# Performance work log

Hardware: AMD Instinct MI355X
Metric: run time of the kernel (lower is better)

## Reference

```python
import jax, jax.numpy as jnp
import numpy as np
import math

B, N, DIM, DEPTH, HEADS, DHEAD = 4, 8192, 256, 4, 8, 32
NB = int(DHEAD * math.log(DHEAD))  # 110 random features (performer_pytorch default)
INNER = HEADS * DHEAD  # 256


def _ortho_proj(rng, nb, d):
    # gaussian orthogonal random matrix, scaling=0 (row norms of a fresh gaussian)
    blocks = []
    for _ in range(-(-nb // d)):
        q, _ = np.linalg.qr(rng.standard_normal((d, d)))
        blocks.append(q.T)
    m = np.concatenate(blocks, 0)[:nb]
    mult = np.linalg.norm(rng.standard_normal((nb, d)), axis=1)
    return (mult[:, None] * m).astype(np.float32)


def setup_inputs() -> dict:
    rng = np.random.default_rng(0)
    p = lambda *s: jnp.asarray((rng.standard_normal(s) * 0.02).astype(np.float32))
    return {
        "x": jnp.asarray(rng.standard_normal((B, N, DIM)).astype(np.float32)),
        "proj": jnp.asarray(np.stack([_ortho_proj(rng, NB, DHEAD) for _ in range(DEPTH)])),
        "ln1_g": jnp.ones((DEPTH, DIM), jnp.float32),
        "ln1_b": jnp.zeros((DEPTH, DIM), jnp.float32),
        "Wq": p(DEPTH, DIM, INNER), "bq": jnp.zeros((DEPTH, INNER), jnp.float32),
        "Wk": p(DEPTH, DIM, INNER), "bk": jnp.zeros((DEPTH, INNER), jnp.float32),
        "Wv": p(DEPTH, DIM, INNER), "bv": jnp.zeros((DEPTH, INNER), jnp.float32),
        "Wo": p(DEPTH, INNER, DIM), "bo": jnp.zeros((DEPTH, DIM), jnp.float32),
        "ln2_g": jnp.ones((DEPTH, DIM), jnp.float32),
        "ln2_b": jnp.zeros((DEPTH, DIM), jnp.float32),
        "Wf1": p(DEPTH, DIM, 4 * DIM), "bf1": jnp.zeros((DEPTH, 4 * DIM), jnp.float32),
        "Wf2": p(DEPTH, 4 * DIM, DIM), "bf2": jnp.zeros((DEPTH, DIM), jnp.float32),
    }


def _ln(x, g, b):
    m = jnp.mean(x, axis=-1, keepdims=True)
    v = jnp.var(x, axis=-1, keepdims=True)
    return (x - m) * jax.lax.rsqrt(v + 1e-5) * g + b


def _softmax_kernel(x, proj, is_query, eps=1e-4):
    # FAVOR+ positive softmax-kernel feature map
    dn = x.shape[-1] ** -0.25
    ratio = proj.shape[0] ** -0.5
    xd = jnp.einsum('bhnd,md->bhnm', x * dn, proj)          # [b,h,n,nb]
    diag = jnp.sum(x * x, axis=-1, keepdims=True) * (0.5 * dn * dn)
    if is_query:
        mx = jnp.max(xd, axis=-1, keepdims=True)
    else:
        mx = jnp.max(xd, axis=(-2, -1), keepdims=True)
    mx = jax.lax.stop_gradient(mx)
    return ratio * (jnp.exp(xd - diag - mx) + eps)


def reference(x, proj, ln1_g, ln1_b, Wq, bq, Wk, bk, Wv, bv, Wo, bo,
              ln2_g, ln2_b, Wf1, bf1, Wf2, bf2):
    b, n, _ = x.shape
    h = x
    for i in range(DEPTH):
        # --- PreNorm FAVOR+ self-attention ---
        y = _ln(h, ln1_g[i], ln1_b[i])
        q = (y @ Wq[i] + bq[i]).reshape(b, n, HEADS, DHEAD).transpose(0, 2, 1, 3)
        k = (y @ Wk[i] + bk[i]).reshape(b, n, HEADS, DHEAD).transpose(0, 2, 1, 3)
        v = (y @ Wv[i] + bv[i]).reshape(b, n, HEADS, DHEAD).transpose(0, 2, 1, 3)
        qp = _softmax_kernel(q, proj[i], True)   # [b,h,n,nb]
        kp = _softmax_kernel(k, proj[i], False)  # [b,h,n,nb]
        d_inv = 1.0 / jnp.einsum('bhnm,bhm->bhn', qp, kp.sum(axis=2))
        ctx = jnp.einsum('bhnm,bhnd->bhmd', kp, v)          # [b,h,nb,d]
        o = jnp.einsum('bhnm,bhmd,bhn->bhnd', qp, ctx, d_inv)
        o = o.transpose(0, 2, 1, 3).reshape(b, n, INNER)
        h = h + o @ Wo[i] + bo[i]
        # --- PreNorm FFN ---
        y = _ln(h, ln2_g[i], ln2_b[i])
        h = h + jax.nn.gelu(y @ Wf1[i] + bf1[i]) @ Wf2[i] + bf2[i]
    return h
```

## Files before the change

### kernel.cpp

```cpp
#include <hip/hip_runtime.h>
#include <math.h>

#define NSEQ 8192
#define BATCH 4
#define DIM 256
#define HEADS 8
#define DHEAD 32
#define NB 110
#define INNER 256
#define FFDIM 1024
#define MROWS (BATCH * NSEQ)
#define BH (BATCH * HEADS)

typedef __attribute__((ext_vector_type(8))) short bf16x8;
typedef __attribute__((ext_vector_type(4))) short bf16x4;
typedef __attribute__((ext_vector_type(4))) float f32x4;

typedef __attribute__((address_space(1))) const void* gas_cvp;
typedef __attribute__((address_space(3))) void* las_vp;

constexpr float c_dn = 0.42044820762685725f;
constexpr float c_diagf = 0.08838834764831845f;
constexpr float c_ratio = 0.09534625892455922f;

__device__ __forceinline__ unsigned short f2b(float f) {
    unsigned u = __float_as_uint(f);
    unsigned r = (u + 0x7FFFu + ((u >> 16) & 1u)) >> 16;
    return (unsigned short)r;
}
__device__ __forceinline__ float b2f(unsigned short u) {
    return __uint_as_float((unsigned)u << 16);
}

__global__ __launch_bounds__(256) void copy4_kernel(const float4* __restrict__ src,
                                                    float4* __restrict__ dst, int n4) {
    int i = blockIdx.x * 256 + threadIdx.x;
    if (i < n4) dst[i] = src[i];
}
__global__ __launch_bounds__(256) void zero_kernel(float* __restrict__ p, int n) {
    int i = blockIdx.x * 256 + threadIdx.x;
    if (i < n) p[i] = 0.0f;
}
__global__ __launch_bounds__(256) void bcat_kernel(const float* __restrict__ bq,
                                                   const float* __restrict__ bk,
                                                   const float* __restrict__ bv,
                                                   float* __restrict__ out) {
    int l = blockIdx.x, t = threadIdx.x;
    out[l * 768 + t] = bq[l * 256 + t];
    out[l * 768 + 256 + t] = bk[l * 256 + t];
    out[l * 768 + 512 + t] = bv[l * 256 + t];
}

__global__ __launch_bounds__(256) void ln_kernel(const float* __restrict__ x,
                                                 const float* __restrict__ g,
                                                 const float* __restrict__ bta,
                                                 unsigned short* __restrict__ y) {
    int wave = threadIdx.x >> 6, lane = threadIdx.x & 63;
    int row = blockIdx.x * 4 + wave;
    const float* xr = x + (size_t)row * DIM;
    float4 v = *(const float4*)(xr + lane * 4);
    float s = v.x + v.y + v.z + v.w;
    float sq = v.x * v.x + v.y * v.y + v.z * v.z + v.w * v.w;
    #pragma unroll
    for (int off = 32; off; off >>= 1) {
        s += __shfl_xor(s, off);
        sq += __shfl_xor(sq, off);
    }
    float mean = s * (1.0f / DIM);
    float var = sq * (1.0f / DIM) - mean * mean;
    float rstd = rsqrtf(var + 1e-5f);
    float4 gg = *(const float4*)(g + lane * 4);
    float4 bb = *(const float4*)(bta + lane * 4);
    bf16x4 o;
    o[0] = (short)f2b((v.x - mean) * rstd * gg.x + bb.x);
    o[1] = (short)f2b((v.y - mean) * rstd * gg.y + bb.y);
    o[2] = (short)f2b((v.z - mean) * rstd * gg.z + bb.z);
    o[3] = (short)f2b((v.w - mean) * rstd * gg.w + bb.w);
    *(bf16x4*)(y + (size_t)row * DIM + lane * 4) = o;
}

__global__ __launch_bounds__(256) void wt_kernel(const float* __restrict__ in,
                                                 unsigned short* __restrict__ out,
                                                 int K, int Nn, int lstride) {
    __shared__ float t32[32][33];
    int l = blockIdx.z;
    const float* inp = in + (size_t)l * K * Nn;
    unsigned short* outp = out + (size_t)l * lstride;
    int k0 = blockIdx.x * 32, n0 = blockIdx.y * 32;
    int tx = threadIdx.x & 31, ty = threadIdx.x >> 5;
    #pragma unroll
    for (int i = 0; i < 4; ++i)
        t32[ty + i * 8][tx] = inp[(size_t)(k0 + ty + i * 8) * Nn + n0 + tx];
    __syncthreads();
    #pragma unroll
    for (int i = 0; i < 4; ++i) {
        int r = ty + i * 8;
        outp[(size_t)(n0 + r) * K + k0 + tx] = f2b(t32[tx][r]);
    }
}

template <int EPI>
__global__ __launch_bounds__(256) void gemm_mfma(const unsigned short* __restrict__ A,
                                                 const unsigned short* __restrict__ Wt,
                                                 const float* __restrict__ bias,
                                                 const float* __restrict__ res,
                                                 void* __restrict__ Cv,
                                                 int Nn, int K) {
    __shared__ __align__(16) unsigned short pool[24576];
    unsigned short* AsP = pool;
    unsigned short* BsP = pool + 12288;
    int tid = threadIdx.x;
    int nwg = gridDim.x * gridDim.y;
    int orig = blockIdx.y * gridDim.x + blockIdx.x;
    int swz = (orig & 7) * (nwg >> 3) + (orig >> 3);
    int m0 = (swz / gridDim.x) * 128, n0 = (swz % gridDim.x) * 128;
    int wave = tid >> 6, lane = tid & 63;
    int wm = (wave >> 1) * 64, wn = (wave & 1) * 64;
    int lr = lane & 15, lg = lane >> 4;
    f32x4 acc[4][4];
    #pragma unroll
    for (int i = 0; i < 4; ++i)
        #pragma unroll
        for (int j = 0; j < 4; ++j) acc[i][j] = (f32x4){0.f, 0.f, 0.f, 0.f};

    int rowS[2], chS[2];
    #pragma unroll
    for (int j = 0; j < 2; ++j) {
        int f = wave * 128 + j * 64 + lane;
        rowS[j] = f >> 2;
        chS[j] = ((f & 3) ^ ((rowS[j] >> 1) & 3)) * 8;
    }
    int rdA[4], rdB[4];
    #pragma unroll
    for (int i = 0; i < 4; ++i) {
        int ra = wm + i * 16 + lr;
        rdA[i] = ra * 32 + (lg ^ ((ra >> 1) & 3)) * 8;
        int rb = wn + i * 16 + lr;
        rdB[i] = rb * 32 + (lg ^ ((rb >> 1) & 3)) * 8;
    }

    const int NT = K >> 5;
    #pragma unroll
    for (int t = 0; t < 2; ++t) {
        #pragma unroll
        for (int j = 0; j < 2; ++j) {
            const unsigned short* srcA = A + (size_t)(m0 + rowS[j]) * K + t * 32 + chS[j];
            __builtin_amdgcn_global_load_lds((gas_cvp)srcA,
                                             (las_vp)(AsP + t * 4096 + wave * 1024 + j * 512), 16, 0, 0);
            const unsigned short* srcB = Wt + (size_t)(n0 + rowS[j]) * K + t * 32 + chS[j];
            __builtin_amdgcn_global_load_lds((gas_cvp)srcB,
                                             (las_vp)(BsP + t * 4096 + wave * 1024 + j * 512), 16, 0, 0);
        }
    }
    int buf = 0;
    for (int kt = 0; kt < NT; ++kt) {
        if (kt + 2 < NT) {
            int nb = (kt + 2) % 3;
            int koff = (kt + 2) * 32;
            #pragma unroll
            for (int j = 0; j < 2; ++j) {
                const unsigned short* srcA = A + (size_t)(m0 + rowS[j]) * K + koff + chS[j];
                __builtin_amdgcn_global_load_lds((gas_cvp)srcA,
                                                 (las_vp)(AsP + nb * 4096 + wave * 1024 + j * 512), 16, 0, 0);
                const unsigned short* srcB = Wt + (size_t)(n0 + rowS[j]) * K + koff + chS[j];
                __builtin_amdgcn_global_load_lds((gas_cvp)srcB,
                                                 (las_vp)(BsP + nb * 4096 + wave * 1024 + j * 512), 16, 0, 0);
            }
        }
        int ahead = NT - 1 - kt;
        if (ahead >= 2)      asm volatile("s_waitcnt vmcnt(8)" ::: "memory");
        else if (ahead == 1) asm volatile("s_waitcnt vmcnt(4)" ::: "memory");
        else                 asm volatile("s_waitcnt vmcnt(0)" ::: "memory");
        __builtin_amdgcn_s_barrier();
        __builtin_amdgcn_sched_barrier(0);
        bf16x8 af[4], bfv[4];
        #pragma unroll
        for (int i = 0; i < 4; ++i) af[i] = *(bf16x8*)&AsP[buf * 4096 + rdA[i]];
        #pragma unroll
        for (int j = 0; j < 4; ++j) bfv[j] = *(bf16x8*)&BsP[buf * 4096 + rdB[j]];
        #pragma unroll
        for (int i = 0; i < 4; ++i)
            #pragma unroll
            for (int j = 0; j < 4; ++j)
                acc[i][j] = __builtin_amdgcn_mfma_f32_16x16x32_bf16(af[i], bfv[j], acc[i][j], 0, 0, 0);
        __builtin_amdgcn_sched_barrier(0);
        __builtin_amdgcn_s_barrier();
        buf = (buf + 1 == 3) ? 0 : buf + 1;
    }

    #pragma unroll
    for (int i = 0; i < 4; ++i) {
        #pragma unroll
        for (int j = 0; j < 4; ++j) {
            int tcol = wn + j * 16 + lr;
            float bv = bias[n0 + tcol];
            #pragma unroll
            for (int r = 0; r < 4; ++r) {
                int trow = wm + i * 16 + lg * 4 + r;
                float c = acc[i][j][r] + bv;
                if (EPI == 2) {
                    float u = c;
                    float t = 1.5957691216057308f * (u + 0.044715f * u * u * u);
                    c = u / (1.0f + __expf(-t));
                }
                pool[trow * 128 + (((tcol >> 3) ^ (trow & 7)) << 3) + (tcol & 7)] = f2b(c);
            }
        }
    }
    __syncthreads();
    #pragma unroll
    for (int cch = 0; cch < 8; ++cch) {
        int g = cch * 256 + tid;
        int row = g >> 4, cc = g & 15;
        bf16x8 val = *(bf16x8*)&pool[row * 128 + ((cc ^ (row & 7)) << 3)];
        int grow = m0 + row;
        int gcol = n0 + cc * 8;
        if (EPI == 3) {
            size_t idx = (size_t)(gcol >> 8) * ((size_t)MROWS * DIM) + (size_t)grow * 256 + (gcol & 255);
            *(bf16x8*)((unsigned short*)Cv + idx) = val;
        } else {
            *(bf16x8*)((unsigned short*)Cv + (size_t)grow * Nn + gcol) = val;
        }
    }
}

template <int DO_LN>
__global__ __launch_bounds__(256) void gemm_ln(const unsigned short* __restrict__ A,
                                               const unsigned short* __restrict__ Wt,
                                               const float* __restrict__ bias,
                                               const float* __restrict__ res,
                                               float* __restrict__ hout,
                                               unsigned short* __restrict__ yout,
                                               const float* __restrict__ gam,
                                               const float* __restrict__ bet,
                                               int K) {
    __shared__ __align__(16) unsigned short As[2][64 * 32];
    __shared__ __align__(16) unsigned short Bs[2][256 * 32];
    int tid = threadIdx.x;
    int nwg = gridDim.y;
    int orig = blockIdx.y;
    int swz = (orig & 7) * (nwg >> 3) + (orig >> 3);
    int m0 = swz * 64;
    int wave = tid >> 6, lane = tid & 63;
    int lr = lane & 15, lg = lane >> 4;

    f32x4 acc[16];
    #pragma unroll
    for (int j = 0; j < 16; ++j) acc[j] = (f32x4){0.f, 0.f, 0.f, 0.f};

    int fA = wave * 64 + lane;
    int rowA = fA >> 2, chA = ((fA & 3) ^ ((rowA >> 1) & 3)) * 8;
    int rowB[4], chB[4];
    #pragma unroll
    for (int j = 0; j < 4; ++j) {
        int f = wave * 256 + j * 64 + lane;
        rowB[j] = f >> 2;
        chB[j] = ((f & 3) ^ ((rowB[j] >> 1) & 3)) * 8;
    }
    int raA = wave * 16 + lr;
    int rdAo = raA * 32 + (lg ^ ((raA >> 1) & 3)) * 8;
    int rdBo[16];
    #pragma unroll
    for (int j = 0; j < 16; ++j) {
        int rb = j * 16 + lr;
        rdBo[j] = rb * 32 + (lg ^ ((rb >> 1) & 3)) * 8;
    }

    const int NT = K >> 5;
    {
        const unsigned short* srcA = A + (size_t)(m0 + rowA) * K + chA;
        __builtin_amdgcn_global_load_lds((gas_cvp)srcA, (las_vp)(&As[0][wave * 512]), 16, 0, 0);
        #pragma unroll
        for (int j = 0; j < 4; ++j) {
            const unsigned short* srcB = Wt + (size_t)rowB[j] * K + chB[j];
            __builtin_amdgcn_global_load_lds((gas_cvp)srcB, (las_vp)(&Bs[0][wave * 2048 + j * 512]), 16, 0, 0);
        }
    }
    for (int kt = 0; kt < NT; ++kt) {
        int cur = kt & 1;
        if (kt + 1 < NT) {
            int nxt = cur ^ 1;
            int koff = (kt + 1) * 32;
            const unsigned short* srcA = A + (size_t)(m0 + rowA) * K + koff + chA;
            __builtin_amdgcn_global_load_lds((gas_cvp)srcA, (las_vp)(&As[nxt][wave * 512]), 16, 0, 0);
            #pragma unroll
            for (int j = 0; j < 4; ++j) {
                const unsigned short* srcB = Wt + (size_t)rowB[j] * K + koff + chB[j];
                __builtin_amdgcn_global_load_lds((gas_cvp)srcB, (las_vp)(&Bs[nxt][wave * 2048 + j * 512]), 16, 0, 0);
            }
            asm volatile("s_waitcnt vmcnt(5)" ::: "memory");
        } else {
            asm volatile("s_waitcnt vmcnt(0)" ::: "memory");
        }
        __builtin_amdgcn_s_barrier();
        __builtin_amdgcn_sched_barrier(0);
        bf16x8 af = *(bf16x8*)&As[cur][rdAo];
        #pragma unroll
        for (int j = 0; j < 16; ++j) {
            bf16x8 bv = *(bf16x8*)&Bs[cur][rdBo[j]];
            acc[j] = __builtin_amdgcn_mfma_f32_16x16x32_bf16(af, bv, acc[j], 0, 0, 0);
        }
        __builtin_amdgcn_sched_barrier(0);
        __builtin_amdgcn_s_barrier();
    }

    float rs[4] = {0.f, 0.f, 0.f, 0.f};
    float rq[4] = {0.f, 0.f, 0.f, 0.f};
    #pragma unroll
    for (int j = 0; j < 16; ++j) {
        int col = j * 16 + lr;
        float bv = bias[col];
        #pragma unroll
        for (int r = 0; r < 4; ++r) {
            int row = m0 + wave * 16 + lg * 4 + r;
            float c = acc[j][r] + bv + res[(size_t)row * 256 + col];
            hout[(size_t)row * 256 + col] = c;
            acc[j][r] = c;
            if (DO_LN) { rs[r] += c; rq[r] += c * c; }
        }
    }
    if (DO_LN) {
        #pragma unroll
        for (int r = 0; r < 4; ++r) {
            float s = rs[r], sq = rq[r];
            s += __shfl_xor(s, 1);  sq += __shfl_xor(sq, 1);
            s += __shfl_xor(s, 2);  sq += __shfl_xor(sq, 2);
            s += __shfl_xor(s, 4);  sq += __shfl_xor(sq, 4);
            s += __shfl_xor(s, 8);  sq += __shfl_xor(sq, 8);
            rs[r] = s; rq[r] = sq;
        }
        #pragma unroll
        for (int r = 0; r < 4; ++r) {
            float mean = rs[r] * (1.0f / 256.0f);
            float var = rq[r] * (1.0f / 256.0f) - mean * mean;
            rs[r] = mean;
            rq[r] = rsqrtf(var + 1e-5f);
        }
        #pragma unroll
        for (int j = 0; j < 16; ++j) {
            int col = j * 16 + lr;
            float gv = gam[col], bb = bet[col];
            #pragma unroll
            for (int r = 0; r < 4; ++r) {
                int row = m0 + wave * 16 + lg * 4 + r;
                float yv = (acc[j][r] - rs[r]) * rq[r] * gv + bb;
                yout[(size_t)row * 256 + col] = f2b(yv);
            }
        }
    }
}

__global__ __launch_bounds__(256) void kmaxg_kernel(const unsigned short* __restrict__ k,
                                                    const float* __restrict__ proj,
                                                    float* __restrict__ partial) {
    __shared__ unsigned short As[128][40];
    __shared__ unsigned short Pj[112][40];
    __shared__ float wmax[4][8];
    int tid = threadIdx.x;
    int r0 = blockIdx.x * 128;
    for (int idx = tid; idx < 112 * 8; idx += 256) {
        int m = idx >> 3, f4 = idx & 7;
        if (m < NB) {
            float4 va = *(const float4*)(proj + m * 32 + f4 * 4);
            bf16x4 pk = {(short)f2b(va.x), (short)f2b(va.y), (short)f2b(va.z), (short)f2b(va.w)};
            *(bf16x4*)&Pj[m][f4 * 4] = pk;
        } else {
            *(bf16x4*)&Pj[m][f4 * 4] = (bf16x4){0, 0, 0, 0};
        }
    }
    int arow = tid >> 1, ahalf = tid & 1;
    const unsigned short* ap = k + (size_t)(r0 + arow) * 32 + ahalf * 16;
    *(bf16x8*)&As[arow][ahalf * 16] = *(const bf16x8*)ap;
    *(bf16x8*)&As[arow][ahalf * 16 + 8] = *(const bf16x8*)(ap + 8);
    __syncthreads();
    int wave = tid >> 6, lane = tid & 63, lr = lane & 15, lg = lane >> 4;
    float mymax[4] = {-1e30f, -1e30f, -1e30f, -1e30f};
    #pragma unroll
    for (int mt = 0; mt < 2; ++mt) {
        bf16x8 af = *(bf16x8*)&As[(2 * wave + mt) * 16 + lr][lg * 8];
        #pragma unroll
        for (int nt = 0; nt < 7; ++nt) {
            bf16x8 bfp = *(bf16x8*)&Pj[nt * 16 + lr][lg * 8];
            f32x4 d = (f32x4){0.f, 0.f, 0.f, 0.f};
            d = __builtin_amdgcn_mfma_f32_16x16x32_bf16(af, bfp, d, 0, 0, 0);
            if (!(nt == 6 && lr >= 14)) {
                #pragma unroll
                for (int r = 0; r < 4; ++r) mymax[r] = fmaxf(mymax[r], d[r]);
            }
        }
    }
    #pragma unroll
    for (int r = 0; r < 4; ++r) {
        float v = mymax[r];
        v = fmaxf(v, __shfl_xor(v, 1));
        v = fmaxf(v, __shfl_xor(v, 2));
        v = fmaxf(v, __shfl_xor(v, 4));
        v = fmaxf(v, __shfl_xor(v, 8));
        v = fmaxf(v, __shfl_xor(v, 32));
        mymax[r] = v;
    }
    if (lane == 0 || lane == 16) {
        int hb = (lane >> 4) & 1;
        #pragma unroll
        for (int r = 0; r < 4; ++r) wmax[wave][4 * hb + r] = mymax[r];
    }
    __syncthreads();
    if (tid < 8) {
        float m = fmaxf(fmaxf(wmax[0][tid], wmax[1][tid]), fmaxf(wmax[2][tid], wmax[3][tid]));
        partial[blockIdx.x * 8 + tid] = m * c_dn;
    }
}

__global__ __launch_bounds__(256) void kreduce_kernel(const float* __restrict__ partial,
                                                      float* __restrict__ kmaxf) {
    __shared__ float wred[4];
    int bh = blockIdx.x, b = bh >> 3, h = bh & 7;
    int tid = threadIdx.x;
    float m = fmaxf(partial[(b * 512 + tid) * 8 + h], partial[(b * 512 + 256 + tid) * 8 + h]);
    #pragma unroll
    for (int off = 32; off; off >>= 1) m = fmaxf(m, __shfl_xor(m, off));
    if ((tid & 63) == 0) wred[tid >> 6] = m;
    __syncthreads();
    if (tid == 0)
        kmaxf[bh] = fmaxf(fmaxf(wred[0], wred[1]), fmaxf(wred[2], wred[3]));
}

__global__ __launch_bounds__(256) void ctxg_kernel(const unsigned short* __restrict__ k,
                                                   const unsigned short* __restrict__ v,
                                                   const float* __restrict__ proj,
                                                   const float* __restrict__ kmaxf,
                                                   float* __restrict__ ctx) {
    __shared__ __align__(16) char pool[34816];
    unsigned short (*As)[40] = (unsigned short(*)[40])pool;
    unsigned short (*KpT)[136] = (unsigned short(*)[136])pool;
    __shared__ unsigned short Pj[112][40];
    __shared__ unsigned short VsT[48][136];
    __shared__ float dg[128];
    int tid = threadIdx.x;
    int bh = blockIdx.y, b = bh >> 3, h = bh & 7;
    int n_base = blockIdx.x * 512;
    float mx = kmaxf[bh];
    for (int idx = tid; idx < 112 * 8; idx += 256) {
        int m = idx >> 3, f4 = idx & 7;
        if (m < NB) {
            float4 va = *(const float4*)(proj + m * 32 + f4 * 4);
            bf16x4 pk = {(short)f2b(va.x), (short)f2b(va.y), (short)f2b(va.z), (short)f2b(va.w)};
            *(bf16x4*)&Pj[m][f4 * 4] = pk;
        } else {
            *(bf16x4*)&Pj[m][f4 * 4] = (bf16x4){0, 0, 0, 0};
        }
    }
    for (int idx = tid; idx < 16 * 136; idx += 256) KpT[112 + idx / 136][idx % 136] = 0;
    for (int idx = tid; idx < 16 * 128; idx += 256) {
        int rr = 32 + (idx >> 7), nn = idx & 127;
        VsT[rr][nn] = (rr == 32) ? (unsigned short)0x3F80 : (unsigned short)0;
    }
    int wave = tid >> 6, lane = tid & 63, lr = lane & 15, lg = lane >> 4;
    int arow = tid >> 1, ahalf = tid & 1;
    f32x4 ctxacc[2][3];
    #pragma unroll
    for (int mt = 0; mt < 2; ++mt)
        #pragma unroll
        for (int nt = 0; nt < 3; ++nt) ctxacc[mt][nt] = (f32x4){0.f, 0.f, 0.f, 0.f};

    for (int ni = 0; ni < 4; ++ni) {
        int n0 = n_base + ni * 128;
        {
            const unsigned short* kp_ = k + ((size_t)(b * NSEQ + n0 + arow) * 256 + h * 32 + ahalf * 16);
            bf16x8 k0 = *(const bf16x8*)kp_;
            bf16x8 k1 = *(const bf16x8*)(kp_ + 8);
            *(bf16x8*)&As[arow][ahalf * 16] = k0;
            *(bf16x8*)&As[arow][ahalf * 16 + 8] = k1;
            float ssq = 0.f;
            #pragma unroll
            for (int e = 0; e < 8; ++e) {
                float a = b2f((unsigned short)k0[e]), bb = b2f((unsigned short)k1[e]);
                ssq += a * a + bb * bb;
            }
            ssq += __shfl_xor(ssq, 1);
            if (ahalf == 0) dg[arow] = ssq * c_diagf;
        }
        #pragma unroll
        for (int it = 0; it < 4; ++it) {
            int idx = it * 256 + tid;
            int nn = idx >> 3, f4 = idx & 7;
            bf16x4 vv = *(const bf16x4*)(v + ((size_t)(b * NSEQ + n0 + nn) * 256 + h * 32 + f4 * 4));
            VsT[f4 * 4 + 0][nn] = (unsigned short)vv[0];
            VsT[f4 * 4 + 1][nn] = (unsigned short)vv[1];
            VsT[f4 * 4 + 2][nn] = (unsigned short)vv[2];
            VsT[f4 * 4 + 3][nn] = (unsigned short)vv[3];
        }
        __syncthreads();
        f32x4 xds[2][7];
        #pragma unroll
        for (int mt = 0; mt < 2; ++mt) {
            bf16x8 af = *(bf16x8*)&As[(2 * wave + mt) * 16 + lr][lg * 8];
            #pragma unroll
            for (int nt = 0; nt < 7; ++nt) {
                bf16x8 bfp = *(bf16x8*)&Pj[nt * 16 + lr][lg * 8];
                f32x4 d = (f32x4){0.f, 0.f, 0.f, 0.f};
                xds[mt][nt] = __builtin_amdgcn_mfma_f32_16x16x32_bf16(af, bfp, d, 0, 0, 0);
            }
        }
        __syncthreads();
        #pragma unroll
        for (int mt = 0; mt < 2; ++mt)
            #pragma unroll
            for (int nt = 0; nt < 7; ++nt) {
                int m = nt * 16 + lr;
                #pragma unroll
                for (int r = 0; r < 4; ++r) {
                    int nn = (2 * wave + mt) * 16 + lg * 4 + r;
                    float kpv = (m < NB) ? c_ratio * (__expf(xds[mt][nt][r] * c_dn - dg[nn] - mx) + 1e-4f) : 0.f;
                    KpT[m][nn] = f2b(kpv);
                }
            }
        __syncthreads();
        #pragma unroll
        for (int ks = 0; ks < 4; ++ks)
            #pragma unroll
            for (int mt = 0; mt < 2; ++mt) {
                bf16x8 af2 = *(bf16x8*)&KpT[(2 * wave + mt) * 16 + lr][ks * 32 + lg * 8];
                #pragma unroll
                for (int nt = 0; nt < 3; ++nt) {
                    bf16x8 bf2v = *(bf16x8*)&VsT[nt * 16 + lr][ks * 32 + lg * 8];
                    ctxacc[mt][nt] = __builtin_amdgcn_mfma_f32_16x16x32_bf16(af2, bf2v, ctxacc[mt][nt], 0, 0, 0);
                }
            }
        __syncthreads();
    }
    #pragma unroll
    for (int mt = 0; mt < 2; ++mt)
        #pragma unroll
        for (int nt = 0; nt < 3; ++nt)
            #pragma unroll
            for (int r = 0; r < 4; ++r) {
                int m = (2 * wave + mt) * 16 + lg * 4 + r;
                atomicAdd(&ctx[((size_t)bh * 128 + m) * 48 + nt * 16 + lr], ctxacc[mt][nt][r]);
            }
}

__global__ __launch_bounds__(256) void og_kernel(const unsigned short* __restrict__ q,
                                                 const float* __restrict__ proj,
                                                 const float* __restrict__ ctx,
                                                 unsigned short* __restrict__ o) {
    __shared__ __align__(16) char pool[34816];
    unsigned short (*As)[40] = (unsigned short(*)[40])pool;
    unsigned short (*Qp)[136] = (unsigned short(*)[136])pool;
    __shared__ unsigned short Pj[112][40];
    __shared__ unsigned short CsT[48][136];
    __shared__ float dg[128];
    int tid = threadIdx.x;
    int bh = blockIdx.x >> 6, b = bh >> 3, h = bh & 7;
    int n0 = (blockIdx.x & 63) * 128;
    for (int idx = tid; idx < 112 * 8; idx += 256) {
        int m = idx >> 3, f4 = idx & 7;
        if (m < NB) {
            float4 va = *(const float4*)(proj + m * 32 + f4 * 4);
            bf16x4 pk = {(short)f2b(va.x), (short)f2b(va.y), (short)f2b(va.z), (short)f2b(va.w)};
            *(bf16x4*)&Pj[m][f4 * 4] = pk;
        } else {
            *(bf16x4*)&Pj[m][f4 * 4] = (bf16x4){0, 0, 0, 0};
        }
    }
    for (int idx = tid; idx < 128 * 12; idx += 256) {
        int m = idx / 12, c4 = idx - m * 12;
        float4 cv = *(const float4*)(ctx + ((size_t)bh * 128 + m) * 48 + c4 * 4);
        CsT[c4 * 4 + 0][m] = f2b(cv.x);
        CsT[c4 * 4 + 1][m] = f2b(cv.y);
        CsT[c4 * 4 + 2][m] = f2b(cv.z);
        CsT[c4 * 4 + 3][m] = f2b(cv.w);
    }
    int arow = tid >> 1, ahalf = tid & 1;
    {
        const unsigned short* qp_ = q + ((size_t)(b * NSEQ + n0 + arow) * 256 + h * 32 + ahalf * 16);
        bf16x8 q0 = *(const bf16x8*)qp_;
        bf16x8 q1 = *(const bf16x8*)(qp_ + 8);
        *(bf16x8*)&As[arow][ahalf * 16] = q0;
        *(bf16x8*)&As[arow][ahalf * 16 + 8] = q1;
        float ssq = 0.f;
        #pragma unroll
        for (int e = 0; e < 8; ++e) {
            float a = b2f((unsigned short)q0[e]), bb = b2f((unsigned short)q1[e]);
            ssq += a * a + bb * bb;
        }
        ssq += __shfl_xor(ssq, 1);
        if (ahalf == 0) dg[arow] = ssq * c_diagf;
    }
    __syncthreads();
    int wave = tid >> 6, lane = tid & 63, lr = lane & 15, lg = lane >> 4;
    f32x4 xds[2][7];
    #pragma unroll
    for (int mt = 0; mt < 2; ++mt) {
        bf16x8 af = *(bf16x8*)&As[(2 * wave + mt) * 16 + lr][lg * 8];
        #pragma unroll
        for (int nt = 0; nt < 7; ++nt) {
            bf16x8 bfp = *(bf16x8*)&Pj[nt * 16 + lr][lg * 8];
            f32x4 d = (f32x4){0.f, 0.f, 0.f, 0.f};
            xds[mt][nt] = __builtin_amdgcn_mfma_f32_16x16x32_bf16(af, bfp, d, 0, 0, 0);
        }
    }
    float rmax[2][4];
    #pragma unroll
    for (int mt = 0; mt < 2; ++mt)
        #pragma unroll
        for (int r = 0; r < 4; ++r) {
            float mv = -1e30f;
            #pragma unroll
            for (int nt = 0; nt < 7; ++nt)
                if (!(nt == 6 && lr >= 14)) mv = fmaxf(mv, xds[mt][nt][r]);
            mv = fmaxf(mv, __shfl_xor(mv, 1));
            mv = fmaxf(mv, __shfl_xor(mv, 2));
            mv = fmaxf(mv, __shfl_xor(mv, 4));
            mv = fmaxf(mv, __shfl_xor(mv, 8));
            rmax[mt][r] = mv;
        }
    __syncthreads();
    #pragma unroll
    for (int mt = 0; mt < 2; ++mt)
        #pragma unroll
        for (int r = 0; r < 4; ++r) {
            int row = (2 * wave + mt) * 16 + lg * 4 + r;
            #pragma unroll
            for (int nt = 0; nt < 7; ++nt) {
                int m = nt * 16 + lr;
                float qpv = (m < NB)
                    ? c_ratio * (__expf((xds[mt][nt][r] - rmax[mt][r]) * c_dn - dg[row]) + 1e-4f)
                    : 0.f;
                Qp[row][m] = f2b(qpv);
            }
            Qp[row][112 + lr] = 0;
        }
    __syncthreads();
    f32x4 oacc[2][3];
    #pragma unroll
    for (int mt = 0; mt < 2; ++mt)
        #pragma unroll
        for (int nt = 0; nt < 3; ++nt) oacc[mt][nt] = (f32x4){0.f, 0.f, 0.f, 0.f};
    #pragma unroll
    for (int ks = 0; ks < 4; ++ks)
        #pragma unroll
        for (int mt = 0; mt < 2; ++mt) {
            bf16x8 af2 = *(bf16x8*)&Qp[(2 * wave + mt) * 16 + lr][ks * 32 + lg * 8];
            #pragma unroll
            for (int nt = 0; nt < 3; ++nt) {
                bf16x8 bf2v = *(bf16x8*)&CsT[nt * 16 + lr][ks * 32 + lg * 8];
                oacc[mt][nt] = __builtin_amdgcn_mfma_f32_16x16x32_bf16(af2, bf2v, oacc[mt][nt], 0, 0, 0);
            }
        }
    #pragma unroll
    for (int mt = 0; mt < 2; ++mt)
        #pragma unroll
        for (int r = 0; r < 4; ++r) {
            int row = (2 * wave + mt) * 16 + lg * 4 + r;
            int n = n0 + row;
            float den = __shfl(oacc[mt][2][r], lane & 48);
            float inv = 1.0f / den;
            size_t base = (size_t)(b * NSEQ + n) * 256 + h * 32;
            o[base + lr] = f2b(oacc[mt][0][r] * inv);
            o[base + 16 + lr] = f2b(oacc[mt][1][r] * inv);
        }
}

extern "C" void kernel_launch(void* const* d_in, const int* in_sizes, int n_in,
                              void* d_out, int out_size, void* d_ws, size_t ws_size,
                              hipStream_t stream) {
    const float* x = (const float*)d_in[0];
    const float* proj = (const float*)d_in[1];
    const float* ln1_g = (const float*)d_in[2];
    const float* ln1_b = (const float*)d_in[3];
    const float* Wq = (const float*)d_in[4];
    const float* bq = (const float*)d_in[5];
    const float* Wk = (const float*)d_in[6];
    const float* bk = (const float*)d_in[7];
    const float* Wv = (const float*)d_in[8];
    const float* bv = (const float*)d_in[9];
    const float* Wo = (const float*)d_in[10];
    const float* bo = (const float*)d_in[11];
    const float* ln2_g = (const float*)d_in[12];
    const float* ln2_b = (const float*)d_in[13];
    const float* Wf1 = (const float*)d_in[14];
    const float* bf1 = (const float*)d_in[15];
    const float* Wf2 = (const float*)d_in[16];
    const float* bf2 = (const float*)d_in[17];

    float* h = (float*)d_out;
    const size_t ACT = (size_t)MROWS * DIM;
    unsigned short* y = (unsigned short*)d_ws;
    unsigned short* q = y + ACT;
    unsigned short* k = q + ACT;
    unsigned short* v = k + ACT;
    unsigned short* mid = v + ACT;
    float* ctx = (float*)(mid + 4 * ACT);
    float* kmaxf = ctx + (size_t)BH * 128 * 48;
    float* partial = kmaxf + 32;
    float* bqkv = partial + 2048 * 8;
    unsigned short* wt = (unsigned short*)(bqkv + 4 * 768);
    unsigned short* o = y;

    const int WT_L = 786432;
    const int CTXN = BH * 128 * 48;

    copy4_kernel<<<(int)(ACT / 4) / 256, 256, 0, stream>>>((const float4*)x, (float4*)h, (int)(ACT / 4));

    wt_kernel<<<dim3(8, 8, 4), 256, 0, stream>>>(Wq, wt + 0, 256, 256, WT_L);
    wt_kernel<<<dim3(8, 8, 4), 256, 0, stream>>>(Wk, wt + 65536, 256, 256, WT_L);
    wt_kernel<<<dim3(8, 8, 4), 256, 0, stream>>>(Wv, wt + 131072, 256, 256, WT_L);
    wt_kernel<<<dim3(8, 8, 4), 256, 0, stream>>>(Wo, wt + 196608, 256, 256, WT_L);
    wt_kernel<<<dim3(8, 32, 4), 256, 0, stream>>>(Wf1, wt + 262144, 256, 1024, WT_L);
    wt_kernel<<<dim3(32, 8, 4), 256, 0, stream>>>(Wf2, wt + 524288, 1024, 256, WT_L);
    bcat_kernel<<<4, 256, 0, stream>>>(bq, bk, bv, bqkv);

    ln_kernel<<<MROWS / 4, 256, 0, stream>>>(h, ln1_g, ln1_b, y);

    for (int i = 0; i < 4; ++i) {
        const float* proj_i = proj + (size_t)i * NB * DHEAD;
        const unsigned short* wl = wt + (size_t)i * WT_L;
        gemm_mfma<3><<<dim3(6, 256), 256, 0, stream>>>(y, wl + 0, bqkv + i * 768, nullptr, q, 768, DIM);

        zero_kernel<<<(CTXN + 255) / 256, 256, 0, stream>>>(ctx, CTXN);
        kmaxg_kernel<<<2048, 256, 0, stream>>>(k, proj_i, partial);
        kreduce_kernel<<<BH, 256, 0, stream>>>(partial, kmaxf);
        ctxg_kernel<<<dim3(16, BH), 256, 0, stream>>>(k, v, proj_i, kmaxf, ctx);
        og_kernel<<<BH * 64, 256, 0, stream>>>(q, proj_i, ctx, o);

        gemm_ln<1><<<dim3(1, MROWS / 64), 256, 0, stream>>>(o, wl + 196608, bo + i * DIM, h, h, y,
                                                            ln2_g + i * DIM, ln2_b + i * DIM, INNER);

        gemm_mfma<2><<<dim3(8, 256), 256, 0, stream>>>(y, wl + 262144, bf1 + i * FFDIM, nullptr, mid, FFDIM, DIM);
        if (i < 3) {
            gemm_ln<1><<<dim3(1, MROWS / 64), 256, 0, stream>>>(mid, wl + 524288, bf2 + i * DIM, h, h, y,
                                                                ln1_g + (i + 1) * DIM, ln1_b + (i + 1) * DIM, FFDIM);
        } else {
            gemm_ln<0><<<dim3(1, MROWS / 64), 256, 0, stream>>>(mid, wl + 524288, bf2 + i * DIM, h, h, nullptr,
                                                                nullptr, nullptr, FFDIM);
        }
    }
}
```

Measured before the change: 850.2 us.

## Store residual stream in bf16 and use double-buffered GEMM staging

Stores the residual stream h as bf16 instead of fp32 between layers. Only the final layer writes fp32 output, and the initial copy becomes an fp32-to-bf16 conversion. This halves residual read/write traffic in the fused GEMM+LN kernels. Separately, the generic MFMA GEMM goes from triple to double buffering in LDS, which lowers LDS use (more occupancy) but gives less prefetch lookahead. Rounding the residual to bf16 each layer adds accumulated precision error.

```diff
diff --git a/kernel.cpp b/kernel.cpp
--- a/kernel.cpp
+++ b/kernel.cpp
@@ -32,10 +32,14 @@
     return __uint_as_float((unsigned)u << 16);
 }
 
-__global__ __launch_bounds__(256) void copy4_kernel(const float4* __restrict__ src,
-                                                    float4* __restrict__ dst, int n4) {
+__global__ __launch_bounds__(256) void cvt_kernel(const float4* __restrict__ src,
+                                                  bf16x4* __restrict__ dst, int n4) {
     int i = blockIdx.x * 256 + threadIdx.x;
-    if (i < n4) dst[i] = src[i];
+    if (i < n4) {
+        float4 v = src[i];
+        bf16x4 o = {(short)f2b(v.x), (short)f2b(v.y), (short)f2b(v.z), (short)f2b(v.w)};
+        dst[i] = o;
+    }
 }
 __global__ __launch_bounds__(256) void zero_kernel(float* __restrict__ p, int n) {
     int i = blockIdx.x * 256 + threadIdx.x;
@@ -103,12 +107,11 @@
 __global__ __launch_bounds__(256) void gemm_mfma(const unsigned short* __restrict__ A,
                                                  const unsigned short* __restrict__ Wt,
                                                  const float* __restrict__ bias,
-                                                 const float* __restrict__ res,
                                                  void* __restrict__ Cv,
                                                  int Nn, int K) {
-    __shared__ __align__(16) unsigned short pool[24576];
+    __shared__ __align__(16) unsigned short pool[16384];
     unsigned short* AsP = pool;
-    unsigned short* BsP = pool + 12288;
+    unsigned short* BsP = pool + 8192;
     int tid = threadIdx.x;
     int nwg = gridDim.x * gridDim.y;
     int orig = blockIdx.y * gridDim.x + blockIdx.x;
@@ -141,43 +144,39 @@
 
     const int NT = K >> 5;
     #pragma unroll
-    for (int t = 0; t < 2; ++t) {
-        #pragma unroll
-        for (int j = 0; j < 2; ++j) {
-            const unsigned short* srcA = A + (size_t)(m0 + rowS[j]) * K + t * 32 + chS[j];
-            __builtin_amdgcn_global_load_lds((gas_cvp)srcA,
-                                             (las_vp)(AsP + t * 4096 + wave * 1024 + j * 512), 16, 0, 0);
-            const unsigned short* srcB = Wt + (size_t)(n0 + rowS[j]) * K + t * 32 + chS[j];
-            __builtin_amdgcn_global_load_lds((gas_cvp)srcB,
-                                             (las_vp)(BsP + t * 4096 + wave * 1024 + j * 512), 16, 0, 0);
-        }
-    }
-    int buf = 0;
+    for (int j = 0; j < 2; ++j) {
+        const unsigned short* srcA = A + (size_t)(m0 + rowS[j]) * K + chS[j];
+        __builtin_amdgcn_global_load_lds((gas_cvp)srcA,
+                                         (las_vp)(AsP + wave * 1024 + j * 512), 16, 0, 0);
+        const unsigned short* srcB = Wt + (size_t)(n0 + rowS[j]) * K + chS[j];
+        __builtin_amdgcn_global_load_lds((gas_cvp)srcB,
+                                         (las_vp)(BsP + wave * 1024 + j * 512), 16, 0, 0);
+    }
     for (int kt = 0; kt < NT; ++kt) {
-        if (kt + 2 < NT) {
-            int nb = (kt + 2) % 3;
-            int koff = (kt + 2) * 32;
+        int cur = kt & 1;
+        if (kt + 1 < NT) {
+            int nxt = cur ^ 1;
+            int koff = (kt + 1) * 32;
             #pragma unroll
             for (int j = 0; j < 2; ++j) {
                 const unsigned short* srcA = A + (size_t)(m0 + rowS[j]) * K + koff + chS[j];
                 __builtin_amdgcn_global_load_lds((gas_cvp)srcA,
-                                                 (las_vp)(AsP + nb * 4096 + wave * 1024 + j * 512), 16, 0, 0);
+                                                 (las_vp)(AsP + nxt * 4096 + wave * 1024 + j * 512), 16, 0, 0);
                 const unsigned short* srcB = Wt + (size_t)(n0 + rowS[j]) * K + koff + chS[j];
                 __builtin_amdgcn_global_load_lds((gas_cvp)srcB,
-                                                 (las_vp)(BsP + nb * 4096 + wave * 1024 + j * 512), 16, 0, 0);
-            }
-        }
-        int ahead = NT - 1 - kt;
-        if (ahead >= 2)      asm volatile("s_waitcnt vmcnt(8)" ::: "memory");
-        else if (ahead == 1) asm volatile("s_waitcnt vmcnt(4)" ::: "memory");
-        else                 asm volatile("s_waitcnt vmcnt(0)" ::: "memory");
+                                                 (las_vp)(BsP + nxt * 4096 + wave * 1024 + j * 512), 16, 0, 0);
+            }
+            asm volatile("s_waitcnt vmcnt(4)" ::: "memory");
+        } else {
+            asm volatile("s_waitcnt vmcnt(0)" ::: "memory");
+        }
         __builtin_amdgcn_s_barrier();
         __builtin_amdgcn_sched_barrier(0);
         bf16x8 af[4], bfv[4];
         #pragma unroll
-        for (int i = 0; i < 4; ++i) af[i] = *(bf16x8*)&AsP[buf * 4096 + rdA[i]];
-        #pragma unroll
-        for (int j = 0; j < 4; ++j) bfv[j] = *(bf16x8*)&BsP[buf * 4096 + rdB[j]];
+        for (int i = 0; i < 4; ++i) af[i] = *(bf16x8*)&AsP[cur * 4096 + rdA[i]];
+        #pragma unroll
+        for (int j = 0; j < 4; ++j) bfv[j] = *(bf16x8*)&BsP[cur * 4096 + rdB[j]];
         #pragma unroll
         for (int i = 0; i < 4; ++i)
             #pragma unroll
@@ -185,7 +184,6 @@
                 acc[i][j] = __builtin_amdgcn_mfma_f32_16x16x32_bf16(af[i], bfv[j], acc[i][j], 0, 0, 0);
         __builtin_amdgcn_sched_barrier(0);
         __builtin_amdgcn_s_barrier();
-        buf = (buf + 1 == 3) ? 0 : buf + 1;
     }
 
     #pragma unroll
@@ -224,12 +222,12 @@
     }
 }
 
-template <int DO_LN>
+template <int DO_LN, int F32OUT>
 __global__ __launch_bounds__(256) void gemm_ln(const unsigned short* __restrict__ A,
                                                const unsigned short* __restrict__ Wt,
                                                const float* __restrict__ bias,
-                                               const float* __restrict__ res,
-                                               float* __restrict__ hout,
+                                               const unsigned short* __restrict__ res,
+                                               void* __restrict__ hout,
                                                unsigned short* __restrict__ yout,
                                                const float* __restrict__ gam,
                                                const float* __restrict__ bet,
@@ -313,8 +311,9 @@
         #pragma unroll
         for (int r = 0; r < 4; ++r) {
             int row = m0 + wave * 16 + lg * 4 + r;
-            float c = acc[j][r] + bv + res[(size_t)row * 256 + col];
-            hout[(size_t)row * 256 + col] = c;
+            float c = acc[j][r] + bv + b2f(res[(size_t)row * 256 + col]);
+            if (F32OUT) ((float*)hout)[(size_t)row * 256 + col] = c;
+            else ((unsigned short*)hout)[(size_t)row * 256 + col] = f2b(c);
             acc[j][r] = c;
             if (DO_LN) { rs[r] += c; rq[r] += c * c; }
         }
@@ -684,14 +683,15 @@
     const float* Wf2 = (const float*)d_in[16];
     const float* bf2 = (const float*)d_in[17];
 
-    float* h = (float*)d_out;
+    float* hf = (float*)d_out;
     const size_t ACT = (size_t)MROWS * DIM;
     unsigned short* y = (unsigned short*)d_ws;
     unsigned short* q = y + ACT;
     unsigned short* k = q + ACT;
     unsigned short* v = k + ACT;
     unsigned short* mid = v + ACT;
-    float* ctx = (float*)(mid + 4 * ACT);
+    unsigned short* hb = mid + 4 * ACT;
+    float* ctx = (float*)(hb + ACT);
     float* kmaxf = ctx + (size_t)BH * 128 * 48;
     float* partial = kmaxf + 32;
     float* bqkv = partial + 2048 * 8;
@@ -701,7 +701,7 @@
     const int WT_L = 786432;
     const int CTXN = BH * 128 * 48;
 
-    copy4_kernel<<<(int)(ACT / 4) / 256, 256, 0, stream>>>((const float4*)x, (float4*)h, (int)(ACT / 4));
+    cvt_kernel<<<(int)(ACT / 4) / 256, 256, 0, stream>>>((const float4*)x, (bf16x4*)hb, (int)(ACT / 4));
 
     wt_kernel<<<dim3(8, 8, 4), 256, 0, stream>>>(Wq, wt + 0, 256, 256, WT_L);
     wt_kernel<<<dim3(8, 8, 4), 256, 0, stream>>>(Wk, wt + 65536, 256, 256, WT_L);
@@ -711,12 +711,12 @@
     wt_kernel<<<dim3(32, 8, 4), 256, 0, stream>>>(Wf2, wt + 524288, 1024, 256, WT_L);
     bcat_kernel<<<4, 256, 0, stream>>>(bq, bk, bv, bqkv);
 
-    ln_kernel<<<MROWS / 4, 256, 0, stream>>>(h, ln1_g, ln1_b, y);
+    ln_kernel<<<MROWS / 4, 256, 0, stream>>>(x, ln1_g, ln1_b, y);
 
     for (int i = 0; i < 4; ++i) {
         const float* proj_i = proj + (size_t)i * NB * DHEAD;
         const unsigned short* wl = wt + (size_t)i * WT_L;
-        gemm_mfma<3><<<dim3(6, 256), 256, 0, stream>>>(y, wl + 0, bqkv + i * 768, nullptr, q, 768, DIM);
+        gemm_mfma<3><<<dim3(6, 256), 256, 0, stream>>>(y, wl + 0, bqkv + i * 768, q, 768, DIM);
 
         zero_kernel<<<(CTXN + 255) / 256, 256, 0, stream>>>(ctx, CTXN);
         kmaxg_kernel<<<2048, 256, 0, stream>>>(k, proj_i, partial);
@@ -724,16 +724,16 @@
         ctxg_kernel<<<dim3(16, BH), 256, 0, stream>>>(k, v, proj_i, kmaxf, ctx);
         og_kernel<<<BH * 64, 256, 0, stream>>>(q, proj_i, ctx, o);
 
-        gemm_ln<1><<<dim3(1, MROWS / 64), 256, 0, stream>>>(o, wl + 196608, bo + i * DIM, h, h, y,
-                                                            ln2_g + i * DIM, ln2_b + i * DIM, INNER);
-
-        gemm_mfma<2><<<dim3(8, 256), 256, 0, stream>>>(y, wl + 262144, bf1 + i * FFDIM, nullptr, mid, FFDIM, DIM);
+        gemm_ln<1, 0><<<dim3(1, MROWS / 64), 256, 0, stream>>>(o, wl + 196608, bo + i * DIM, hb, hb, y,
+                                                               ln2_g + i * DIM, ln2_b + i * DIM, INNER);
+
+        gemm_mfma<2><<<dim3(8, 256), 256, 0, stream>>>(y, wl + 262144, bf1 + i * FFDIM, mid, FFDIM, DIM);
         if (i < 3) {
-            gemm_ln<1><<<dim3(1, MROWS / 64), 256, 0, stream>>>(mid, wl + 524288, bf2 + i * DIM, h, h, y,
-                                                                ln1_g + (i + 1) * DIM, ln1_b + (i + 1) * DIM, FFDIM);
+            gemm_ln<1, 0><<<dim3(1, MROWS / 64), 256, 0, stream>>>(mid, wl + 524288, bf2 + i * DIM, hb, hb, y,
+                                                                   ln1_g + (i + 1) * DIM, ln1_b + (i + 1) * DIM, FFDIM);
         } else {
-            gemm_ln<0><<<dim3(1, MROWS / 64), 256, 0, stream>>>(mid, wl + 524288, bf2 + i * DIM, h, h, nullptr,
-                                                                nullptr, nullptr, FFDIM);
-        }
-    }
-}
+            gemm_ln<0, 1><<<dim3(1, MROWS / 64), 256, 0, stream>>>(mid, wl + 524288, bf2 + i * DIM, hb, hf, nullptr,
+                                                                   nullptr, nullptr, FFDIM);
+        }
+    }
+}
```

Measured after the change: 803.2 us. -5.5%, faster.
